# Performance work log

Measured on AMD Instinct MI355X. Metric: run time of the kernel, lower is better.

## Reference

```python
import jax, jax.numpy as jnp
import numpy as np
import math
from jax import lax

K = 3  # kernel size for every layer


def _get_size(h, w, stride, ceil_mode):
    ah, aw = h - (K - 1), w - (K - 1)
    if ceil_mode:
        return math.ceil(ah / stride), math.ceil(aw / stride)
    return ah // stride, aw // stride


def _sample(h, w, stride, ceil_mode, mask_out, rng):
    """Replicates SConv2dAvg.sample: random in-stride offsets per output cell,
    plus bottom-up input mask = union of 3x3 windows of selected positions
    where the downstream mask is active."""
    ah, aw = h - (K - 1), w - (K - 1)
    oh, ow = _get_size(h, w, stride, ceil_mode)
    selh = rng.integers(0, stride, (oh, ow)).astype(np.int32)
    selw = rng.integers(0, stride, (oh, ow)).astype(np.int32)
    resth, restw = oh * stride - ah, ow * stride - aw
    if resth > 0:
        selh[-1, :] = selh[-1, :] % resth
    if restw > 0:
        selw[:, -1] = selw[:, -1] % restw
    ph = selh + (np.arange(oh) * stride)[:, None]  # conv-grid row of selected window
    pw = selw + (np.arange(ow) * stride)[None, :]
    mask_in = np.zeros((h, w), np.int32)
    ys = ph[mask_out == 1]
    xs = pw[mask_out == 1]
    for dy in range(K):
        for dx in range(K):
            mask_in[ys + dy, xs + dx] = 1
    return selh, selw, mask_in


def setup_inputs() -> dict:
    key = jax.random.key(0)
    rng = np.random.default_rng(0)
    B, H0, W0 = 64, 132, 132
    ks = jax.random.split(key, 9)
    x = jax.random.normal(ks[0], (B, 3, H0, W0), jnp.float32)

    def conv_params(kw_, kb_, cout, cin):
        bound = 1.0 / np.sqrt(cin * K * K)
        w = jax.random.uniform(kw_, (cout, cin, K, K), jnp.float32, -bound, bound)
        b = jax.random.uniform(kb_, (cout,), jnp.float32, -bound, bound)
        return w, b

    w1, b1 = conv_params(ks[1], ks[2], 200, 3)
    w2, b2 = conv_params(ks[3], ks[4], 400, 200)
    w3, b3 = conv_params(ks[5], ks[6], 800, 400)
    w4, b4 = conv_params(ks[7], ks[8], 10, 800)

    h1, wd1 = _get_size(H0, W0, 2, False)   # 65,65
    h2, wd2 = _get_size(h1, wd1, 2, False)  # 31,31
    h3, wd3 = _get_size(h2, wd2, 2, True)   # 15,15
    mask3 = np.ones((h3, wd3), np.int32)
    selh3, selw3, mask2 = _sample(h2, wd2, 2, True, mask3, rng)
    selh2, selw2, mask1 = _sample(h1, wd1, 2, False, mask2, rng)
    selh1, selw1, _ = _sample(H0, W0, 2, False, mask1, rng)

    j = jnp.asarray
    return {
        "x": x,
        "w1": w1, "b1": b1, "w2": w2, "b2": b2,
        "w3": w3, "b3": b3, "w4": w4, "b4": b4,
        "selh1": j(selh1), "selw1": j(selw1), "mask1": j(mask1),
        "selh2": j(selh2), "selw2": j(selw2), "mask2": j(mask2),
        "selh3": j(selh3), "selw3": j(selw3), "mask3": j(mask3),
    }


def _sconv_stoch(x, weight, bias, selh, selw, mask, stride):
    """Stochastic strided conv: per output cell, evaluate the 3x3 valid conv at a
    randomly selected position inside its stride x stride block; zero unmasked
    cells (they were never computed), then add bias everywhere."""
    oh, ow = selh.shape
    kh, kw = weight.shape[2], weight.shape[3]
    ph = selh + jnp.arange(oh, dtype=selh.dtype)[:, None] * stride  # (oh,ow)
    pw = selw + jnp.arange(ow, dtype=selw.dtype)[None, :] * stride
    ih = ph[:, :, None, None] + jnp.arange(kh)[None, None, :, None]  # (oh,ow,kh,kw)
    iw = pw[:, :, None, None] + jnp.arange(kw)[None, None, None, :]
    patches = x[:, :, ih, iw]  # (B, Cin, oh, ow, kh, kw)
    out = jnp.einsum('bchwij,ocij->bohw', patches, weight)
    out = jnp.where(mask[None, None] == 1, out, jnp.zeros((), out.dtype))
    return out + bias[None, :, None, None]


def reference(x, w1, b1, w2, b2, w3, b3, w4, b4,
              selh1, selw1, mask1, selh2, selw2, mask2, selh3, selw3, mask3):
    out = jax.nn.relu(_sconv_stoch(x, w1, b1, selh1, selw1, mask1, 2))
    out = jax.nn.relu(_sconv_stoch(out, w2, b2, selh2, selw2, mask2, 2))
    out = jax.nn.relu(_sconv_stoch(out, w3, b3, selh3, selw3, mask3, 2))
    out = lax.conv_general_dilated(out, w4, (1, 1), 'VALID') + b4[None, :, None, None]
    return out.reshape(out.shape[0], -1)
```

## Files before the change

kernel.cpp:

```cpp
#include <hip/hip_runtime.h>
#include <hip/hip_bf16.h>

using bf16 = __hip_bfloat16;
using short8 = __attribute__((ext_vector_type(8))) short;
using sh4 = __attribute__((ext_vector_type(4))) short;
using f32x4 = __attribute__((ext_vector_type(4))) float;

__device__ __align__(16) bf16 g_wp1[16 * 3 * 512];
__device__ __align__(16) bf16 g_wp2[63 * 32 * 512];
__device__ __align__(16) bf16 g_wp3[2 * 117 * 32 * 512];
__device__ __align__(16) bf16 g_wp4[1 * 225 * 512];

__device__ int g_list1[4225];
__device__ int g_list2[961];
__device__ int g_list3[225];
__device__ int g_cnt[3];


__global__ __launch_bounds__(256) void k_pack1(const float* __restrict__ w) {
  int el = blockIdx.x * 256 + threadIdx.x;
  if (el >= 16 * 3 * 512) return;
  int j = el & 7, lane = (el >> 3) & 63, rest = el >> 9;
  int kt = rest % 3, mt = rest / 3;
  int m = mt * 16 + (lane & 15);
  int k = kt * 32 + ((lane >> 4) * 8) + j;
  int chunk = k >> 3, c = k & 7;
  float val = 0.f;
  if (m < 200 && chunk < 9 && c < 3) val = w[((size_t)m * 3 + c) * 9 + chunk];
  g_wp1[el] = __float2bfloat16(val);
}
template <int CIN, int SUBT, int COUT, int KT>
__device__ __forceinline__ void pack_kmaj(const float* __restrict__ w,
                                          bf16* __restrict__ dst, int total) {
  int el = blockIdx.x * 256 + threadIdx.x;
  if (el >= total) return;
  int j = el & 7, lane = (el >> 3) & 63, ti = el >> 9;
  int half = ti / (KT * 32);
  int r2 = ti - half * (KT * 32);
  int kt = r2 >> 5, mtl = r2 & 31;
  int mt = half * 32 + mtl;
  int chunk = kt / SUBT, cc = kt - chunk * SUBT;
  int m = mt * 16 + (lane & 15);
  int c = cc * 32 + ((lane >> 4) * 8) + j;
  float val = 0.f;
  if (m < COUT && c < CIN) val = w[((size_t)m * CIN + c) * 9 + chunk];
  dst[el] = __float2bfloat16(val);
}
__global__ __launch_bounds__(256) void k_pack2(const float* __restrict__ w) {
  pack_kmaj<200, 7, 400, 63>(w, g_wp2, 63 * 32 * 512);
}
__global__ __launch_bounds__(256) void k_pack3(const float* __restrict__ w) {
  pack_kmaj<400, 13, 800, 117>(w, g_wp3, 2 * 117 * 32 * 512);
}
__global__ __launch_bounds__(256) void k_pack4(const float* __restrict__ w) {
  int el = blockIdx.x * 256 + threadIdx.x;
  if (el >= 225 * 512) return;
  int j = el & 7, lane = (el >> 3) & 63, rest = el >> 9;
  int kt = rest % 225;
  int chunk = kt / 25, cc = kt - chunk * 25;
  int m = lane & 15;
  int c = cc * 32 + ((lane >> 4) * 8) + j;
  float val = 0.f;
  if (m < 10 && c < 800) val = w[((size_t)m * 800 + c) * 9 + chunk];
  g_wp4[el] = __float2bfloat16(val);
}

__global__ __launch_bounds__(256) void k_compact(const int* __restrict__ m1,
                                                 const int* __restrict__ m2,
                                                 const int* __restrict__ m3) {
  const int which = blockIdx.x;
  const int* m = which == 0 ? m1 : (which == 1 ? m2 : m3);
  int* lst = which == 0 ? g_list1 : (which == 1 ? g_list2 : g_list3);
  const int n = which == 0 ? 4225 : (which == 1 ? 961 : 225);
  const int per = (n + 255) / 256;
  const int lo = threadIdx.x * per;
  const int hi = lo + per < n ? lo + per : n;
  __shared__ int cnt[256];
  __shared__ int off[256];
  int c = 0;
  for (int i = lo; i < hi; ++i) c += (m[i] != 0);
  cnt[threadIdx.x] = c;
  __syncthreads();
  if (threadIdx.x == 0) {
    int s = 0;
    for (int t = 0; t < 256; ++t) { off[t] = s; s += cnt[t]; }
    g_cnt[which] = s;
  }
  __syncthreads();
  int o = off[threadIdx.x];
  for (int i = lo; i < hi; ++i)
    if (m[i] != 0) lst[o++] = i;
}

template <int COUT>
__global__ __launch_bounds__(256) void k_fill_off(const int* __restrict__ mask,
                                                  const float* __restrict__ bias,
                                                  bf16* __restrict__ out_t) {
  constexpr int NFULL = (COUT / 32) * 32;
  constexpr int TW = COUT - NFULL;
  constexpr int TD = TW ? TW * 16 : 1;
  const int pos = blockIdx.x;
  if (mask[pos] != 0) return;
  bf16* base = out_t + (size_t)pos * 64 * COUT;
  for (int idx = threadIdx.x; idx < 64 * COUT / 8; idx += 256) {
    const int e0 = idx * 8;
    int ch0;
    if (e0 < NFULL * 64) {
      const int cc = e0 >> 11;
      const int r = e0 & 2047;
      const int lq = (r >> 7) & 3;
      ch0 = cc * 32 + lq * 8;
    } else {
      const int r = e0 - NFULL * 64;
      const int r2 = r - (r / TD) * TD;
      const int mq = (TW == 16) ? (r2 >> 7) : 0;
      ch0 = NFULL + mq * 8;
    }
    short8 s;
#pragma unroll
    for (int j = 0; j < 8; ++j) {
      float v = bias[ch0 + j];
      v = v > 0.f ? v : 0.f;
      bf16 h = __float2bfloat16(v);
      s[j] = *reinterpret_cast<short*>(&h);
    }
    *reinterpret_cast<short8*>(base + e0) = s;
  }
}

__global__ __launch_bounds__(256) void k_fill_xt(float* __restrict__ p, int n4) {
  int i = blockIdx.x * 256 + threadIdx.x;
  if (i < n4) reinterpret_cast<float4*>(p)[i] = float4{0.f, 0.f, 0.f, 0.f};
}
__global__ __launch_bounds__(256) void k_zero_out(float* __restrict__ p) {
  int i = blockIdx.x * 256 + threadIdx.x;
  if (i < 64 * 10 * 13 * 13) p[i] = 0.f;
}

__global__ __launch_bounds__(256) void k_transpose_x(const float* __restrict__ x,
                                                     bf16* __restrict__ xt) {
  int idx = blockIdx.x * 256 + threadIdx.x;
  constexpr int N = 64 * 3 * 132 * 132;
  if (idx >= N) return;
  int w = idx % 132;
  int t = idx / 132;
  int h = t % 132;
  t /= 132;
  int c = t % 3;
  int b = t / 3;
  xt[((size_t)(h * 132 + w) * 64 + b) * 8 + c] = __float2bfloat16(x[idx]);
}

template <int COUT, int MT>
__device__ __forceinline__ void epilogue_frag(f32x4 (&acc)[MT][4], int pos,
                                              int mt0, int q, int nl,
                                              const float* bias, bf16* out_t) {
  constexpr int NFULL = (COUT / 32) * 32;
  constexpr int TW = COUT - NFULL;
  bf16* cell = out_t + (size_t)pos * (COUT * 64);
#pragma unroll
  for (int ms = 0; ms < MT; ++ms) {
    const int T = mt0 + ms;
    const int mbase = T * 16 + q * 4;
    if (mbase < COUT) {
      const float4 bv = *reinterpret_cast<const float4*>(bias + mbase);
#pragma unroll
      for (int t = 0; t < 4; ++t) {
        sh4 s;
#pragma unroll
        for (int r = 0; r < 4; ++r) {
          float vv = acc[ms][t][r] + ((const float*)&bv)[r];
          vv = vv > 0.f ? vv : 0.f;
          bf16 h = __float2bfloat16(vv);
          s[r] = *reinterpret_cast<short*>(&h);
        }
        size_t el;
        if (mbase < NFULL) {
          el = ((size_t)((mbase >> 5) * 4 + t) * 64 +
                (((mbase >> 3) & 3) * 16 + nl)) * 8 + (mbase & 7);
        } else {
          el = (size_t)NFULL * 64 + t * (TW * 16) +
               ((TW == 16) ? (((mbase >> 3) & 1) * 128) : 0) + nl * 8 +
               (mbase & 7);
        }
        *reinterpret_cast<sh4*>(cell + el) = s;
      }
    }
  }
}

template <int CINW, int COUT, int WIN, int OW, int KTILES, int MT>
__device__ __forceinline__ void sconv_body_div(
    const bf16* __restrict__ in_t, const bf16* __restrict__ wp,
    const float* __restrict__ bias, const int* __restrict__ selh,
    const int* __restrict__ selw, const int* __restrict__ list, int which,
    bf16* __restrict__ out_t) {
  const int bid = blockIdx.x;
  if (bid >= g_cnt[which]) return;
  const int pos = list[bid];
  const int tid = threadIdx.x;
  const int lane = tid & 63;
  const int wv = tid >> 6;
  const int nl = lane & 15;
  const int q = lane >> 4;
  const int mt0 = blockIdx.y * (4 * MT) + wv * MT;
  f32x4 acc[MT][4] = {};
  const int y = pos / OW, xq = pos % OW;
  const int ph = selh[pos] + 2 * y;
  const int pw = selw[pos] + 2 * xq;
  const short8* ap = reinterpret_cast<const short8*>(wp);
#pragma unroll
  for (int kt = 0; kt < KTILES; ++kt) {
    int k = kt * 32 + q * 8;
    int chunk = (int)((unsigned)k / (unsigned)CINW);
    int c = k - chunk * CINW;
    if (chunk > 8) { chunk = 8; c = 0; }
    const int di = (chunk * 342) >> 10;
    const int dj = chunk - di * 3;
    const bf16* bp =
        in_t + ((size_t)((ph + di) * WIN + (pw + dj)) * 64 + nl) * CINW + c;
    short8 Bf[4];
#pragma unroll
    for (int t = 0; t < 4; ++t)
      Bf[t] = *reinterpret_cast<const short8*>(bp + (size_t)t * 16 * CINW);
    short8 Af[MT];
#pragma unroll
    for (int ms = 0; ms < MT; ++ms)
      Af[ms] = ap[((size_t)(mt0 + ms) * KTILES + kt) * 64 + lane];
#pragma unroll
    for (int ms = 0; ms < MT; ++ms)
#pragma unroll
      for (int t = 0; t < 4; ++t)
        acc[ms][t] =
            __builtin_amdgcn_mfma_f32_16x16x32_bf16(Af[ms], Bf[t], acc[ms][t], 0, 0, 0);
  }
  epilogue_frag<COUT, MT>(acc, pos, mt0, q, nl, bias, out_t);
}

template <int CIN, int SUBT, int COUT, int WIN, int OW>
__device__ __forceinline__ void sconv_body_pipe(
    const bf16* __restrict__ in_t, const bf16* __restrict__ wp,
    const float* __restrict__ bias, const int* __restrict__ selh,
    const int* __restrict__ selw, const int* __restrict__ list, int which,
    int bid, int myt, bf16* __restrict__ out_t) {
  constexpr int MT = 4;
  constexpr int KTILES = 9 * SUBT;
  constexpr int NFC = CIN / 32;
  constexpr int TIN = CIN - NFC * 32;
  __shared__ __align__(16) bf16 Ab[3][32 * 512];
  __shared__ __align__(16) bf16 Bb[3][2 * 2048];
  const int cnt = g_cnt[which];
  if (2 * bid >= cnt) return;
  const int p0 = list[2 * bid];
  const int p1 = list[2 * bid + 1 < cnt ? 2 * bid + 1 : cnt - 1];
  const int tid = threadIdx.x;
  const int lane = tid & 63;
  const int wv = tid >> 6;
  const int nl = lane & 15;
  const int q = lane >> 4;
  const int y0 = p0 / OW, x0 = p0 % OW;
  const int y1 = p1 / OW, x1 = p1 % OW;
  const int ph0 = selh[p0] + 2 * y0, pw0 = selw[p0] + 2 * x0;
  const int ph1 = selh[p1] + 2 * y1, pw1 = selw[p1] + 2 * x1;

  auto cellp = [&](int ph, int pw, int chunk) -> const bf16* {
    const int di = (chunk * 342) >> 10;
    const int dj = chunk - di * 3;
    return in_t + (size_t)((ph + di) * WIN + (pw + dj)) * (CIN * 64);
  };

  int scc = 0, sch = 0;
  const bf16* scell0 = cellp(ph0, pw0, 0);
  const bf16* scell1 = cellp(ph1, pw1, 0);

  auto stage = [&](int b) {
    const int kt = sch * SUBT + scc;
    const bf16* asrc = wp + (((size_t)kt * 32 + wv * 4) * 64 + lane) * 8;
#pragma unroll
    for (int i = 0; i < 4; ++i) {
      __builtin_amdgcn_global_load_lds(
          (const __attribute__((address_space(1))) void*)(asrc + (size_t)i * 512),
          (__attribute__((address_space(3))) void*)(&Ab[b][(wv * 4 + i) * 512 +
                                                           lane * 8]),
          16, 0, 0);
    }
    const int j = wv & 3;
    const bf16* cell = (wv >> 2) ? scell1 : scell0;
    int boff;
    if (scc < NFC) {
      boff = (scc * 4 + j) * 512;
    } else {
      int jj = (j * 512 < TIN * 64) ? j : 0;
      boff = NFC * 2048 + jj * 512;
    }
    __builtin_amdgcn_global_load_lds(
        (const __attribute__((address_space(1))) void*)(cell + boff + lane * 8),
        (__attribute__((address_space(3))) void*)(&Bb[b][(wv >> 2) * 2048 +
                                                         j * 512 + lane * 8]),
        16, 0, 0);
    if (++scc == SUBT) {
      scc = 0;
      if (++sch > 8) sch = 8;
      scell0 = cellp(ph0, pw0, sch);
      scell1 = cellp(ph1, pw1, sch);
    }
  };

  f32x4 acc0[MT][4] = {};
  f32x4 acc1[MT][4] = {};

  stage(0);
  stage(1);

  int buf = 0, ccC = 0;
  for (int kt = 0; kt < KTILES; ++kt) {
    __builtin_amdgcn_sched_barrier(0);
    if (kt == KTILES - 1)
      asm volatile("s_waitcnt vmcnt(0)");
    else
      asm volatile("s_waitcnt vmcnt(5)");
    __builtin_amdgcn_sched_barrier(0);
    __builtin_amdgcn_s_barrier();
    __builtin_amdgcn_sched_barrier(0);

    short8 Af[MT];
#pragma unroll
    for (int ms = 0; ms < MT; ++ms)
      Af[ms] = *reinterpret_cast<const short8*>(
          &Ab[buf][(wv * 4 + ms) * 512 + lane * 8]);
    short8 Bf0[4], Bf1[4];
    if (ccC != SUBT - 1) {
#pragma unroll
      for (int t = 0; t < 4; ++t) {
        Bf0[t] = *reinterpret_cast<const short8*>(&Bb[buf][t * 512 + lane * 8]);
        Bf1[t] = *reinterpret_cast<const short8*>(
            &Bb[buf][2048 + t * 512 + lane * 8]);
      }
    } else if (TIN == 8) {
#pragma unroll
      for (int t = 0; t < 4; ++t) {
        Bf0[t] = *reinterpret_cast<const short8*>(&Bb[buf][t * 128 + nl * 8]);
        Bf1[t] =
            *reinterpret_cast<const short8*>(&Bb[buf][2048 + t * 128 + nl * 8]);
      }
    } else {
#pragma unroll
      for (int t = 0; t < 4; ++t) {
        Bf0[t] = *reinterpret_cast<const short8*>(
            &Bb[buf][t * 256 + (q & 1) * 128 + nl * 8]);
        Bf1[t] = *reinterpret_cast<const short8*>(
            &Bb[buf][2048 + t * 256 + (q & 1) * 128 + nl * 8]);
      }
    }
#pragma unroll
    for (int ms = 0; ms < MT; ++ms)
#pragma unroll
      for (int t = 0; t < 4; ++t) {
        acc0[ms][t] = __builtin_amdgcn_mfma_f32_16x16x32_bf16(Af[ms], Bf0[t],
                                                              acc0[ms][t], 0, 0, 0);
        acc1[ms][t] = __builtin_amdgcn_mfma_f32_16x16x32_bf16(Af[ms], Bf1[t],
                                                              acc1[ms][t], 0, 0, 0);
      }
    __builtin_amdgcn_sched_barrier(0);
    if (kt + 2 < KTILES) {
      int sb = buf + 2;
      if (sb >= 3) sb -= 3;
      stage(sb);
    }
    if (++ccC == SUBT) ccC = 0;
    if (++buf == 3) buf = 0;
  }
  const int mt0 = myt * 32 + wv * MT;
  epilogue_frag<COUT, MT>(acc0, p0, mt0, q, nl, bias, out_t);
  epilogue_frag<COUT, MT>(acc1, p1, mt0, q, nl, bias, out_t);
}

__global__ __launch_bounds__(256) void k_sconv1(
    const bf16* __restrict__ in_t, const float* __restrict__ bias,
    const int* __restrict__ selh, const int* __restrict__ selw,
    bf16* __restrict__ out_t) {
  sconv_body_div<8, 200, 132, 65, 3, 4>(in_t, g_wp1, bias, selh, selw, g_list1, 0,
                                        out_t);
}
__global__ __launch_bounds__(512, 1) void k_sconv2(
    const bf16* __restrict__ in_t, const float* __restrict__ bias,
    const int* __restrict__ selh, const int* __restrict__ selw,
    bf16* __restrict__ out_t) {
  sconv_body_pipe<200, 7, 400, 65, 31>(in_t, g_wp2, bias, selh, selw, g_list2, 1,
                                       blockIdx.x, 0, out_t);
}
__global__ __launch_bounds__(512, 1) void k_sconv3(
    const bf16* __restrict__ in_t, const float* __restrict__ bias,
    const int* __restrict__ selh, const int* __restrict__ selw,
    bf16* __restrict__ out_t) {
  const int id = blockIdx.x;
  const int xcd = id & 7;
  const int yhalf = xcd >> 2;
  const int slot = (id >> 3) * 4 + (xcd & 3);
  sconv_body_pipe<400, 13, 800, 31, 15>(in_t, g_wp3 + (size_t)yhalf * 117 * 32 * 512,
                                        bias, selh, selw, g_list3, 2, slot, yhalf,
                                        out_t);
}

__global__ __launch_bounds__(256) void k_conv4m(
    const bf16* __restrict__ in_t,
    const float* __restrict__ bias,
    float* __restrict__ out) {
  const int pos = blockIdx.x;
  const int y = pos / 13, x = pos % 13;
  const int tid = threadIdx.x;
  const int lane = tid & 63;
  const int wv = tid >> 6;
  const int nl = lane & 15;
  const int q = lane >> 4;
  const int kslice = blockIdx.y * 4 + wv;
  __shared__ f32x4 Racc[4][4][64];
  f32x4 acc[4] = {};
  const short8* ap = reinterpret_cast<const short8*>(g_wp4);
  for (int kt = kslice; kt < 225; kt += 16) {
    const int chunk = kt / 25;
    const int cc = kt - chunk * 25;
    const int di = chunk / 3, dj = chunk - di * 3;
    const bf16* cell = in_t + (size_t)((y + di) * 15 + (x + dj)) * (800 * 64);
    short8 A0 = ap[(size_t)kt * 64 + lane];
    short8 Bf[4];
#pragma unroll
    for (int t = 0; t < 4; ++t)
      Bf[t] = *reinterpret_cast<const short8*>(
          cell + ((size_t)(cc * 4 + t) * 64 + lane) * 8);
#pragma unroll
    for (int t = 0; t < 4; ++t)
      acc[t] = __builtin_amdgcn_mfma_f32_16x16x32_bf16(A0, Bf[t], acc[t], 0, 0, 0);
  }
#pragma unroll
  for (int t = 0; t < 4; ++t) Racc[wv][t][lane] = acc[t];
  __syncthreads();
  if (wv == 0) {
    const int rowb = q * 4;
#pragma unroll
    for (int t = 0; t < 4; ++t) {
      f32x4 s = Racc[0][t][lane];
#pragma unroll
      for (int w2 = 1; w2 < 4; ++w2) {
        f32x4 o = Racc[w2][t][lane];
#pragma unroll
        for (int r = 0; r < 4; ++r) s[r] += o[r];
      }
      const int n = t * 16 + nl;
#pragma unroll
      for (int r = 0; r < 4; ++r) {
        const int m = rowb + r;
        if (m < 10) {
          float v = s[r] + (blockIdx.y == 0 ? bias[m] : 0.f);
          atomicAdd(&out[(((size_t)n * 10 + m) * 13 + y) * 13 + x], v);
        }
      }
    }
  }
}

extern "C" void kernel_launch(void* const* d_in, const int* in_sizes, int n_in,
                              void* d_out, int out_size, void* d_ws, size_t ws_size,
                              hipStream_t stream) {
  const float* x  = (const float*)d_in[0];
  const float* w1 = (const float*)d_in[1];
  const float* b1 = (const float*)d_in[2];
  const float* w2 = (const float*)d_in[3];
  const float* b2 = (const float*)d_in[4];
  const float* w3 = (const float*)d_in[5];
  const float* b3 = (const float*)d_in[6];
  const float* w4 = (const float*)d_in[7];
  const float* b4 = (const float*)d_in[8];
  const int* selh1 = (const int*)d_in[9];
  const int* selw1 = (const int*)d_in[10];
  const int* mask1 = (const int*)d_in[11];
  const int* selh2 = (const int*)d_in[12];
  const int* selw2 = (const int*)d_in[13];
  const int* mask2 = (const int*)d_in[14];
  const int* selh3 = (const int*)d_in[15];
  const int* selw3 = (const int*)d_in[16];
  const int* mask3 = (const int*)d_in[17];

  char* ws = (char*)d_ws;
  bf16* o1t = (bf16*)(ws);
  bf16* xt  = (bf16*)(ws + 108160000);
  bf16* o2t = (bf16*)(ws + 108160000);
  bf16* o3t = (bf16*)(ws);

  k_pack1<<<dim3((16 * 3 * 512 + 255) / 256), dim3(256), 0, stream>>>(w1);
  k_pack2<<<dim3((63 * 32 * 512 + 255) / 256), dim3(256), 0, stream>>>(w2);
  k_pack3<<<dim3((2 * 117 * 32 * 512 + 255) / 256), dim3(256), 0, stream>>>(w3);
  k_pack4<<<dim3((225 * 512 + 255) / 256), dim3(256), 0, stream>>>(w4);
  k_compact<<<dim3(3), dim3(256), 0, stream>>>(mask1, mask2, mask3);
  k_fill_xt<<<dim3((2230272 + 255) / 256), dim3(256), 0, stream>>>((float*)xt, 2230272);
  k_transpose_x<<<dim3((64 * 3 * 132 * 132 + 255) / 256), dim3(256), 0, stream>>>(x, xt);
  k_zero_out<<<dim3((64 * 10 * 13 * 13 + 255) / 256), dim3(256), 0, stream>>>(
      (float*)d_out);

  k_fill_off<200><<<dim3(4225), dim3(256), 0, stream>>>(mask1, b1, o1t);
  k_sconv1<<<dim3(4225, 1), dim3(256), 0, stream>>>(xt, b1, selh1, selw1, o1t);

  k_fill_off<400><<<dim3(961), dim3(256), 0, stream>>>(mask2, b2, o2t);
  k_sconv2<<<dim3(481, 1), dim3(512), 0, stream>>>(o1t, b2, selh2, selw2, o2t);

  k_fill_off<800><<<dim3(225), dim3(256), 0, stream>>>(mask3, b3, o3t);
  k_sconv3<<<dim3(232, 1), dim3(512), 0, stream>>>(o2t, b3, selh3, selw3, o3t);

  k_conv4m<<<dim3(13 * 13, 4), dim3(256), 0, stream>>>(o3t, b4, (float*)d_out);
}
```

Baseline: 466.3 us.

## Split pipelined sconv work across 16 waves, one output position per wave

Layer-2 and layer-3 stochastic convs now launch 1024-thread blocks with 16 waves instead of 8. Each wave accumulates a single output position instead of two, which halves accumulator registers. Weight-tile staging is spread over all 16 waves, while only the first 8 still stage the input cells, and the per-wave vmcnt waits are adjusted to match. MFMA sections are wrapped in s_setprio to favour compute waves. The intent is more latency hiding and lower register pressure, at the cost of more barrier participants and LDS fragment reads duplicated across waves.

```diff
diff --git a/kernel.cpp b/kernel.cpp
--- a/kernel.cpp
+++ b/kernel.cpp
@@ -256,6 +256,8 @@
   const int tid = threadIdx.x;
   const int lane = tid & 63;
   const int wv = tid >> 6;
+  const int msl = wv & 7;
+  const int pp = wv >> 3;
   const int nl = lane & 15;
   const int q = lane >> 4;
   const int y0 = p0 / OW, x0 = p0 % OW;
@@ -275,29 +277,31 @@
 
   auto stage = [&](int b) {
     const int kt = sch * SUBT + scc;
-    const bf16* asrc = wp + (((size_t)kt * 32 + wv * 4) * 64 + lane) * 8;
-#pragma unroll
-    for (int i = 0; i < 4; ++i) {
+    const bf16* asrc = wp + ((size_t)kt * 32 + wv * 2) * 512 + lane * 8;
+#pragma unroll
+    for (int i = 0; i < 2; ++i) {
       __builtin_amdgcn_global_load_lds(
           (const __attribute__((address_space(1))) void*)(asrc + (size_t)i * 512),
-          (__attribute__((address_space(3))) void*)(&Ab[b][(wv * 4 + i) * 512 +
+          (__attribute__((address_space(3))) void*)(&Ab[b][(wv * 2 + i) * 512 +
                                                            lane * 8]),
           16, 0, 0);
     }
-    const int j = wv & 3;
-    const bf16* cell = (wv >> 2) ? scell1 : scell0;
-    int boff;
-    if (scc < NFC) {
-      boff = (scc * 4 + j) * 512;
-    } else {
-      int jj = (j * 512 < TIN * 64) ? j : 0;
-      boff = NFC * 2048 + jj * 512;
-    }
-    __builtin_amdgcn_global_load_lds(
-        (const __attribute__((address_space(1))) void*)(cell + boff + lane * 8),
-        (__attribute__((address_space(3))) void*)(&Bb[b][(wv >> 2) * 2048 +
-                                                         j * 512 + lane * 8]),
-        16, 0, 0);
+    if (wv < 8) {
+      const int j = wv & 3;
+      const bf16* cell = (wv >> 2) ? scell1 : scell0;
+      int boff;
+      if (scc < NFC) {
+        boff = (scc * 4 + j) * 512;
+      } else {
+        int jj = (j * 512 < TIN * 64) ? j : 0;
+        boff = NFC * 2048 + jj * 512;
+      }
+      __builtin_amdgcn_global_load_lds(
+          (const __attribute__((address_space(1))) void*)(cell + boff + lane * 8),
+          (__attribute__((address_space(3))) void*)(&Bb[b][(wv >> 2) * 2048 +
+                                                           j * 512 + lane * 8]),
+          16, 0, 0);
+    }
     if (++scc == SUBT) {
       scc = 0;
       if (++sch > 8) sch = 8;
@@ -306,8 +310,7 @@
     }
   };
 
-  f32x4 acc0[MT][4] = {};
-  f32x4 acc1[MT][4] = {};
+  f32x4 acc[MT][4] = {};
 
   stage(0);
   stage(1);
@@ -315,10 +318,13 @@
   int buf = 0, ccC = 0;
   for (int kt = 0; kt < KTILES; ++kt) {
     __builtin_amdgcn_sched_barrier(0);
-    if (kt == KTILES - 1)
+    if (kt == KTILES - 1) {
       asm volatile("s_waitcnt vmcnt(0)");
-    else
-      asm volatile("s_waitcnt vmcnt(5)");
+    } else if (wv < 8) {
+      asm volatile("s_waitcnt vmcnt(3)");
+    } else {
+      asm volatile("s_waitcnt vmcnt(2)");
+    }
     __builtin_amdgcn_sched_barrier(0);
     __builtin_amdgcn_s_barrier();
     __builtin_amdgcn_sched_barrier(0);
@@ -327,40 +333,32 @@
 #pragma unroll
     for (int ms = 0; ms < MT; ++ms)
       Af[ms] = *reinterpret_cast<const short8*>(
-          &Ab[buf][(wv * 4 + ms) * 512 + lane * 8]);
-    short8 Bf0[4], Bf1[4];
+          &Ab[buf][(msl * 4 + ms) * 512 + lane * 8]);
+    short8 Bf[4];
     if (ccC != SUBT - 1) {
 #pragma unroll
-      for (int t = 0; t < 4; ++t) {
-        Bf0[t] = *reinterpret_cast<const short8*>(&Bb[buf][t * 512 + lane * 8]);
-        Bf1[t] = *reinterpret_cast<const short8*>(
-            &Bb[buf][2048 + t * 512 + lane * 8]);
-      }
+      for (int t = 0; t < 4; ++t)
+        Bf[t] = *reinterpret_cast<const short8*>(
+            &Bb[buf][pp * 2048 + t * 512 + lane * 8]);
     } else if (TIN == 8) {
 #pragma unroll
-      for (int t = 0; t < 4; ++t) {
-        Bf0[t] = *reinterpret_cast<const short8*>(&Bb[buf][t * 128 + nl * 8]);
-        Bf1[t] =
-            *reinterpret_cast<const short8*>(&Bb[buf][2048 + t * 128 + nl * 8]);
-      }
+      for (int t = 0; t < 4; ++t)
+        Bf[t] = *reinterpret_cast<const short8*>(
+            &Bb[buf][pp * 2048 + t * 128 + nl * 8]);
     } else {
 #pragma unroll
-      for (int t = 0; t < 4; ++t) {
-        Bf0[t] = *reinterpret_cast<const short8*>(
-            &Bb[buf][t * 256 + (q & 1) * 128 + nl * 8]);
-        Bf1[t] = *reinterpret_cast<const short8*>(
-            &Bb[buf][2048 + t * 256 + (q & 1) * 128 + nl * 8]);
-      }
-    }
+      for (int t = 0; t < 4; ++t)
+        Bf[t] = *reinterpret_cast<const short8*>(
+            &Bb[buf][pp * 2048 + t * 256 + (q & 1) * 128 + nl * 8]);
+    }
+    __builtin_amdgcn_s_setprio(1);
 #pragma unroll
     for (int ms = 0; ms < MT; ++ms)
 #pragma unroll
-      for (int t = 0; t < 4; ++t) {
-        acc0[ms][t] = __builtin_amdgcn_mfma_f32_16x16x32_bf16(Af[ms], Bf0[t],
-                                                              acc0[ms][t], 0, 0, 0);
-        acc1[ms][t] = __builtin_amdgcn_mfma_f32_16x16x32_bf16(Af[ms], Bf1[t],
-                                                              acc1[ms][t], 0, 0, 0);
-      }
+      for (int t = 0; t < 4; ++t)
+        acc[ms][t] = __builtin_amdgcn_mfma_f32_16x16x32_bf16(Af[ms], Bf[t],
+                                                             acc[ms][t], 0, 0, 0);
+    __builtin_amdgcn_s_setprio(0);
     __builtin_amdgcn_sched_barrier(0);
     if (kt + 2 < KTILES) {
       int sb = buf + 2;
@@ -370,9 +368,8 @@
     if (++ccC == SUBT) ccC = 0;
     if (++buf == 3) buf = 0;
   }
-  const int mt0 = myt * 32 + wv * MT;
-  epilogue_frag<COUT, MT>(acc0, p0, mt0, q, nl, bias, out_t);
-  epilogue_frag<COUT, MT>(acc1, p1, mt0, q, nl, bias, out_t);
+  const int mt0 = myt * 32 + msl * MT;
+  epilogue_frag<COUT, MT>(acc, pp ? p1 : p0, mt0, q, nl, bias, out_t);
 }
 
 __global__ __launch_bounds__(256) void k_sconv1(
@@ -382,14 +379,14 @@
   sconv_body_div<8, 200, 132, 65, 3, 4>(in_t, g_wp1, bias, selh, selw, g_list1, 0,
                                         out_t);
 }
-__global__ __launch_bounds__(512, 1) void k_sconv2(
+__global__ __launch_bounds__(1024, 4) void k_sconv2(
     const bf16* __restrict__ in_t, const float* __restrict__ bias,
     const int* __restrict__ selh, const int* __restrict__ selw,
     bf16* __restrict__ out_t) {
   sconv_body_pipe<200, 7, 400, 65, 31>(in_t, g_wp2, bias, selh, selw, g_list2, 1,
                                        blockIdx.x, 0, out_t);
 }
-__global__ __launch_bounds__(512, 1) void k_sconv3(
+__global__ __launch_bounds__(1024, 4) void k_sconv3(
     const bf16* __restrict__ in_t, const float* __restrict__ bias,
     const int* __restrict__ selh, const int* __restrict__ selw,
     bf16* __restrict__ out_t) {
@@ -501,10 +498,10 @@
   k_sconv1<<<dim3(4225, 1), dim3(256), 0, stream>>>(xt, b1, selh1, selw1, o1t);
 
   k_fill_off<400><<<dim3(961), dim3(256), 0, stream>>>(mask2, b2, o2t);
-  k_sconv2<<<dim3(481, 1), dim3(512), 0, stream>>>(o1t, b2, selh2, selw2, o2t);
+  k_sconv2<<<dim3(481, 1), dim3(1024), 0, stream>>>(o1t, b2, selh2, selw2, o2t);
 
   k_fill_off<800><<<dim3(225), dim3(256), 0, stream>>>(mask3, b3, o3t);
-  k_sconv3<<<dim3(232, 1), dim3(512), 0, stream>>>(o2t, b3, selh3, selw3, o3t);
+  k_sconv3<<<dim3(232, 1), dim3(1024), 0, stream>>>(o2t, b3, selh3, selw3, o3t);
 
   k_conv4m<<<dim3(13 * 13, 4), dim3(256), 0, stream>>>(o3t, b4, (float*)d_out);
 }
```

Result: faster. 435.0 us (median of 2 runs) (-6.7%).
